# Kernel tuning notes

Measured on AMD Instinct MI355X. Metric: run time of the kernel, lower is better.

The kernel has to match this reference:

```python
import jax, jax.numpy as jnp
import numpy as np

B, L, D, KD, H = 4, 2048, 512, 64, 8


def _dequant(w_int, scale, zp):
    # per-tensor asymmetric dequantization: (q - zero_point) * scale
    return (w_int.astype(jnp.float32) - zp) * scale


def setup_inputs() -> dict:
    key = jax.random.key(0)
    ks = jax.random.split(key, 20)
    inp = {
        'query': jax.random.normal(ks[0], (B, L, D), jnp.float32),
        'key':   jax.random.normal(ks[1], (B, L, D), jnp.float32),
        'value': jax.random.normal(ks[2], (B, L, D), jnp.float32),
        'wq_q': jax.random.randint(ks[3], (D, KD, H), 0, 127, jnp.int32),
        'wk_q': jax.random.randint(ks[4], (D, KD, H), 0, 127, jnp.int32),
        'wv_q': jax.random.randint(ks[5], (D, KD, H), 0, 127, jnp.int32),
        'wo_q': jax.random.randint(ks[6], (KD * H, D), 0, 127, jnp.int32),
        'bq': jax.random.normal(ks[7], (KD, H), jnp.float32) * 0.02,
        'bk': jax.random.normal(ks[8], (KD, H), jnp.float32) * 0.02,
        'bv': jax.random.normal(ks[9], (KD, H), jnp.float32) * 0.02,
        'bo': jax.random.normal(ks[10], (D,), jnp.float32) * 0.02,
        'scale_q': jax.random.uniform(ks[11], (), jnp.float32, 0.001, 0.01),
        'scale_k': jax.random.uniform(ks[12], (), jnp.float32, 0.001, 0.01),
        'scale_v': jax.random.uniform(ks[13], (), jnp.float32, 0.001, 0.01),
        'scale_o': jax.random.uniform(ks[14], (), jnp.float32, 0.001, 0.01),
        'zp_q': jax.random.uniform(ks[15], (), jnp.float32, 50.0, 70.0),
        'zp_k': jax.random.uniform(ks[16], (), jnp.float32, 50.0, 70.0),
        'zp_v': jax.random.uniform(ks[17], (), jnp.float32, 50.0, 70.0),
        'zp_o': jax.random.uniform(ks[18], (), jnp.float32, 50.0, 70.0),
    }
    return inp


def reference(query, key, value, wq_q, wk_q, wv_q, wo_q, bq, bk, bv, bo,
              scale_q, scale_k, scale_v, scale_o, zp_q, zp_k, zp_v, zp_o):
    # Dequantize int8 weights (quantized-inference path of the layer)
    wq = _dequant(wq_q, scale_q, zp_q)  # (D, KD, H)
    wk = _dequant(wk_q, scale_k, zp_k)
    wv = _dequant(wv_q, scale_v, zp_v)
    wo = _dequant(wo_q, scale_o, zp_o)  # (KD*H, D)

    q = jnp.einsum('bij,jkh->bikh', query, wq) + bq  # (B, L, KD, H)
    k = jnp.einsum('bij,jkh->bikh', key,   wk) + bk
    v = jnp.einsum('bij,jkh->bikh', value, wv) + bv

    # scores: contract over key_dim -> (B, Lq, Lk, H)
    scores = jnp.einsum('bidh,bjdh->bijh', q, k) / jnp.sqrt(jnp.float32(KD))
    # tf softmax over axis=-2 of bikh == key axis (axis 2 here)
    attn = jax.nn.softmax(scores, axis=2)
    out = jnp.einsum('bijh,bjdh->bidh', attn, v)  # (B, L, KD, H)
    out = out.reshape(out.shape[0], out.shape[1], KD * H)  # flatten (d,h) row-major, same as tf.reshape
    return jnp.matmul(out, wo) + bo
```

## Files before the change

kernel.cpp:

```cpp
#include <hip/hip_runtime.h>
#include <math.h>
#include <stdint.h>

#define BB 4
#define LL 2048
#define DD 512
#define KDIM 64
#define HH 8

typedef _Float16 f16;
typedef f16 f16x8 __attribute__((ext_vector_type(8)));
typedef f16 f16x4v __attribute__((ext_vector_type(4)));
typedef float f32x4 __attribute__((ext_vector_type(4)));

__device__ __forceinline__ int swz(int x) { return x ^ (((x >> 7) & 7) << 4); }

__device__ __forceinline__ void gload16(const void* g, void* l) {
    __builtin_amdgcn_global_load_lds(
        (const __attribute__((address_space(1))) void*)g,
        (__attribute__((address_space(3))) void*)l, 16, 0, 0);
}

__device__ __forceinline__ void wait_barrier() {
    asm volatile("s_waitcnt vmcnt(0)" ::: "memory");
    __builtin_amdgcn_s_barrier();
}

__global__ __launch_bounds__(256)
void prep_all(const int* __restrict__ w0, const int* __restrict__ w1,
              const int* __restrict__ w2, const int* __restrict__ w3,
              const float* s0, const float* s1, const float* s2, const float* s3,
              const float* z0, const float* z1, const float* z2, const float* z3,
              f16* o0, f16* o1, f16* o2, f16* o3)
{
    __shared__ float t[32][33];
    const int zi = blockIdx.z;
    const int* W = zi == 0 ? w0 : zi == 1 ? w1 : zi == 2 ? w2 : w3;
    const float sc = *(zi == 0 ? s0 : zi == 1 ? s1 : zi == 2 ? s2 : s3);
    const float zp = *(zi == 0 ? z0 : zi == 1 ? z1 : zi == 2 ? z2 : z3);
    f16* WT = zi == 0 ? o0 : zi == 1 ? o1 : zi == 2 ? o2 : o3;
    const int n0 = blockIdx.x * 32, k0 = blockIdx.y * 32;
    const int x = threadIdx.x & 31, y = threadIdx.x >> 5;
    #pragma unroll
    for (int i = 0; i < 32; i += 8)
        t[y + i][x] = ((float)W[(size_t)(k0 + y + i) * DD + n0 + x] - zp) * sc;
    __syncthreads();
    if (zi == 3) {
        const int k = k0 + x;
        const int kp = (k & 7) * 64 + (k >> 3);
        #pragma unroll
        for (int i = 0; i < 32; i += 8)
            WT[(size_t)(n0 + y + i) * DD + kp] = (f16)t[x][y + i];
    } else {
        #pragma unroll
        for (int i = 0; i < 32; i += 8)
            WT[(size_t)(n0 + y + i) * DD + k0 + x] = (f16)t[x][y + i];
    }
}

__global__ __launch_bounds__(256)
void cast_all(const float* __restrict__ q, const float* __restrict__ k,
              const float* __restrict__ v, f16* oq, f16* ok, f16* ov)
{
    const int yi = blockIdx.y;
    const float* in = yi == 0 ? q : yi == 1 ? k : v;
    f16* out = yi == 0 ? oq : yi == 1 ? ok : ov;
    const int i = (blockIdx.x * 256 + threadIdx.x) * 4;
    float4 x = *(const float4*)(in + i);
    f16x4v o = {(f16)x.x, (f16)x.y, (f16)x.z, (f16)x.w};
    *(f16x4v*)(out + i) = o;
}

template<int EPI>
__device__ __forceinline__
void gemm_body(char* As, char* Bs, const f16* __restrict__ A,
               const f16* __restrict__ BT, const float* __restrict__ bias,
               void* __restrict__ OutP)
{
    const int tid = threadIdx.x, lane = tid & 63, wid = tid >> 6;
    const int g = lane >> 4, ql = lane & 15;
    const int wm = wid >> 1, wn = wid & 1;
    const int bid = blockIdx.x;
    const int sb = (bid & 7) * 32 + (bid >> 3);
    const int rowBase = (sb >> 2) * 128, colBase = (sb & 3) * 128;

    auto stage = [&](int p, int buf) {
        const int kt = p * 32;
        #pragma unroll
        for (int i = 0; i < 2; ++i) {
            const int xl = i * 4096 + wid * 1024 + lane * 16;
            const int xs = swz(xl);
            const int r = xs >> 6, cb = xs & 63;
            const char* asrc;
            if (EPI == 1) {
                const int m = rowBase + r, b = m >> 11, qq = m & 2047;
                const int kp = kt * 2 + cb;
                asrc = (const char*)A +
                       (((size_t)((b * 8 + (kp >> 7)) * 2048 + qq)) << 7) + (kp & 127);
            } else {
                asrc = (const char*)(A + (size_t)(rowBase + r) * DD + kt) + cb;
            }
            gload16(asrc, As + buf * 8192 + xl);
            gload16((const char*)(BT + (size_t)(colBase + r) * DD + kt) + cb,
                    Bs + buf * 8192 + xl);
        }
    };

    const f32x4 zero = {0.f, 0.f, 0.f, 0.f};
    f32x4 acc[4][4];
    #pragma unroll
    for (int i = 0; i < 4; ++i)
        #pragma unroll
        for (int j = 0; j < 4; ++j) acc[i][j] = zero;

    stage(0, 0);

    for (int p = 0; p < 16; ++p) {
        const int buf = p & 1;
        wait_barrier();
        if (p < 15) stage(p + 1, buf ^ 1);
        const char* as = As + buf * 8192;
        const char* bs = Bs + buf * 8192;
        f16x8 af[4], bf[4];
        #pragma unroll
        for (int mf = 0; mf < 4; ++mf)
            af[mf] = *(const f16x8*)(as + swz((wm * 64 + mf * 16 + ql) * 64 + g * 16));
        #pragma unroll
        for (int nf = 0; nf < 4; ++nf)
            bf[nf] = *(const f16x8*)(bs + swz((wn * 64 + nf * 16 + ql) * 64 + g * 16));
        __builtin_amdgcn_s_setprio(1);
        #pragma unroll
        for (int mf = 0; mf < 4; ++mf)
            #pragma unroll
            for (int nf = 0; nf < 4; ++nf)
                acc[mf][nf] = __builtin_amdgcn_mfma_f32_16x16x32_f16(af[mf], bf[nf], acc[mf][nf], 0, 0, 0);
        __builtin_amdgcn_s_setprio(0);
    }

    #pragma unroll
    for (int nf = 0; nf < 4; ++nf) {
        const int n = colBase + wn * 64 + nf * 16 + ql;
        const float bn = bias[n];
        #pragma unroll
        for (int mf = 0; mf < 4; ++mf) {
            const int m0 = rowBase + wm * 64 + mf * 16 + g * 4;
            if (EPI == 2) {
                const int b = m0 >> 11, l0 = m0 & 2047;
                const int kd = n >> 3, hh = n & 7;
                f16x4v o = {(f16)(acc[mf][nf][0] + bn), (f16)(acc[mf][nf][1] + bn),
                            (f16)(acc[mf][nf][2] + bn), (f16)(acc[mf][nf][3] + bn)};
                *(f16x4v*)((f16*)OutP + ((size_t)(b * HH + hh) * KDIM + kd) * LL + l0) = o;
            } else {
                #pragma unroll
                for (int r = 0; r < 4; ++r) {
                    const int m = m0 + r;
                    const float v = acc[mf][nf][r] + bn;
                    if (EPI == 0) {
                        const int b = m >> 11, lr = m & 2047;
                        const int kd = n >> 3, hh = n & 7;
                        ((f16*)OutP)[((size_t)(b * HH + hh) * LL + lr) * KDIM + kd] = (f16)v;
                    } else {
                        ((float*)OutP)[(size_t)m * DD + n] = v;
                    }
                }
            }
        }
    }
}

__global__ __launch_bounds__(256)
void gemm_qkv(const f16* Xq, const f16* Xk, const f16* Xv,
              const f16* WTq, const f16* WTk, const f16* WTv,
              const float* bq, const float* bk, const float* bv,
              f16* Qh, f16* Kh, f16* VhT)
{
    __shared__ __align__(16) char As[2 * 128 * 32 * 2];
    __shared__ __align__(16) char Bs[2 * 128 * 32 * 2];
    const int z = blockIdx.z;
    if (z == 0)      gemm_body<0>(As, Bs, Xq, WTq, bq, Qh);
    else if (z == 1) gemm_body<0>(As, Bs, Xk, WTk, bk, Kh);
    else             gemm_body<2>(As, Bs, Xv, WTv, bv, VhT);
}

__global__ __launch_bounds__(256)
void gemm_out(const f16* A, const f16* BT, const float* bias, float* Out)
{
    __shared__ __align__(16) char As[2 * 128 * 32 * 2];
    __shared__ __align__(16) char Bs[2 * 128 * 32 * 2];
    gemm_body<1>(As, Bs, A, BT, bias, Out);
}

__global__ __launch_bounds__(256, 4)
void attn_f16(const f16* __restrict__ Qh, const f16* __restrict__ Kh,
              const f16* __restrict__ VhT, f16* __restrict__ Ob)
{
    __shared__ __align__(16) char k_s[2][64 * 128];
    __shared__ __align__(16) char v_s[2][64 * 128];
    __shared__ __align__(16) char p_s[4 * 2048];

    const int tid = threadIdx.x, lane = tid & 63, wid = tid >> 6;
    const int g = lane >> 4, ql = lane & 15;
    char* pw = p_s + wid * 2048;

    const int bid = blockIdx.x;
    const int sb = (bid & 7) * 128 + (bid >> 3);
    const int qt = sb & 31, bh = sb >> 5;

    const f16*  Qb = Qh + (size_t)bh * LL * KDIM;
    const char* Kb = (const char*)(Kh + (size_t)bh * LL * KDIM);
    const char* Vb = (const char*)(VhT + (size_t)bh * KDIM * LL);
    const int q0 = qt * 64 + wid * 16;

    auto stage = [&](int t, int buf) {
        const int kv = t * 64;
        #pragma unroll
        for (int i = 0; i < 2; ++i) {
            const int xl = i * 4096 + wid * 1024 + lane * 16;
            const int xs = swz(xl);
            gload16(Kb + (size_t)kv * 128 + xs, k_s[buf] + xl);
            gload16(Vb + (size_t)(xs >> 7) * (LL * 2) + (size_t)kv * 2 + (xs & 127),
                    v_s[buf] + xl);
        }
    };

    stage(0, 0);

    const f16 qscale = (f16)(0.125f * 1.44269504089f);
    f16x8 qfr[2];
    #pragma unroll
    for (int kb = 0; kb < 2; ++kb) {
        qfr[kb] = *(const f16x8*)(Qb + (size_t)(q0 + ql) * KDIM + kb * 32 + g * 8);
        qfr[kb] *= qscale;
    }

    const f32x4 zero = {0.f, 0.f, 0.f, 0.f};
    f32x4 acc[4];
    #pragma unroll
    for (int n = 0; n < 4; ++n) acc[n] = zero;
    float m_r = -1e30f, l_r = 0.f;

    for (int t = 0; t < 32; ++t) {
        const int buf = t & 1;
        wait_barrier();
        if (t < 31) stage(t + 1, buf ^ 1);
        const char* ks = k_s[buf];
        const char* vs = v_s[buf];

        f32x4 s[4];
        __builtin_amdgcn_s_setprio(1);
        #pragma unroll
        for (int kf = 0; kf < 4; ++kf) {
            f16x8 kfr0 = *(const f16x8*)(ks + swz((kf * 16 + ql) * 128 + g * 16));
            f16x8 kfr1 = *(const f16x8*)(ks + swz((kf * 16 + ql) * 128 + 64 + g * 16));
            f32x4 z = zero;
            z = __builtin_amdgcn_mfma_f32_16x16x32_f16(kfr0, qfr[0], z, 0, 0, 0);
            z = __builtin_amdgcn_mfma_f32_16x16x32_f16(kfr1, qfr[1], z, 0, 0, 0);
            s[kf] = z;
        }
        __builtin_amdgcn_s_setprio(0);

        float mx = s[0][0];
        #pragma unroll
        for (int kf = 0; kf < 4; ++kf)
            #pragma unroll
            for (int r = 0; r < 4; ++r) mx = fmaxf(mx, s[kf][r]);
        mx = fmaxf(mx, __shfl_xor(mx, 16));
        mx = fmaxf(mx, __shfl_xor(mx, 32));
        if (__any(mx > m_r + 8.f)) {
            const float mnew = fmaxf(m_r, mx);
            const float fsc = exp2f(m_r - mnew);
            m_r = mnew;
            l_r *= fsc;
            #pragma unroll
            for (int n = 0; n < 4; ++n) acc[n] *= fsc;
        }
        float ps = 0.f;
        #pragma unroll
        for (int kf = 0; kf < 4; ++kf) {
            const float p0 = exp2f(s[kf][0] - m_r);
            const float p1 = exp2f(s[kf][1] - m_r);
            const float p2 = exp2f(s[kf][2] - m_r);
            const float p3 = exp2f(s[kf][3] - m_r);
            ps += (p0 + p1) + (p2 + p3);
            f16x4v pk = {(f16)p0, (f16)p1, (f16)p2, (f16)p3};
            *(f16x4v*)(pw + swz(ql * 128 + kf * 32 + g * 8)) = pk;
        }
        l_r += ps;

        __builtin_amdgcn_s_setprio(1);
        #pragma unroll
        for (int kb = 0; kb < 2; ++kb) {
            f16x8 pf = *(const f16x8*)(pw + swz(ql * 128 + kb * 64 + g * 16));
            #pragma unroll
            for (int n = 0; n < 4; ++n) {
                f16x8 vf = *(const f16x8*)(vs + swz((n * 16 + ql) * 128
                                                    + kb * 64 + g * 16));
                acc[n] = __builtin_amdgcn_mfma_f32_16x16x32_f16(vf, pf, acc[n], 0, 0, 0);
            }
        }
        __builtin_amdgcn_s_setprio(0);
    }

    l_r += __shfl_xor(l_r, 16);
    l_r += __shfl_xor(l_r, 32);
    const float inv = 1.f / l_r;
    const int q = q0 + ql;
    f16* orow = Ob + ((size_t)bh * LL + q) * KDIM;
    #pragma unroll
    for (int n = 0; n < 4; ++n) {
        f16x4v o = {(f16)(acc[n][0] * inv), (f16)(acc[n][1] * inv),
                    (f16)(acc[n][2] * inv), (f16)(acc[n][3] * inv)};
        *(f16x4v*)(orow + n * 16 + g * 4) = o;
    }
}

extern "C" void kernel_launch(void* const* d_in, const int* in_sizes, int n_in,
                              void* d_out, int out_size, void* d_ws, size_t ws_size,
                              hipStream_t stream)
{
    const float* query = (const float*)d_in[0];
    const float* key   = (const float*)d_in[1];
    const float* value = (const float*)d_in[2];
    const int* wq = (const int*)d_in[3];
    const int* wk = (const int*)d_in[4];
    const int* wv = (const int*)d_in[5];
    const int* wo = (const int*)d_in[6];
    const float* bq = (const float*)d_in[7];
    const float* bk = (const float*)d_in[8];
    const float* bv = (const float*)d_in[9];
    const float* bo = (const float*)d_in[10];
    const float* scale_q = (const float*)d_in[11];
    const float* scale_k = (const float*)d_in[12];
    const float* scale_v = (const float*)d_in[13];
    const float* scale_o = (const float*)d_in[14];
    const float* zp_q = (const float*)d_in[15];
    const float* zp_k = (const float*)d_in[16];
    const float* zp_v = (const float*)d_in[17];
    const float* zp_o = (const float*)d_in[18];

    const size_t MD = (size_t)BB * LL * DD;
    const size_t WT_SZ = (size_t)DD * DD;

    f16* Xq  = (f16*)d_ws;
    f16* Xk  = Xq + MD;
    f16* Xv  = Xk + MD;
    f16* WTq = Xv + MD;
    f16* WTk = WTq + WT_SZ;
    f16* WTv = WTk + WT_SZ;
    f16* WTo = WTv + WT_SZ;
    f16* Qh  = WTo + WT_SZ;
    f16* Kh  = Qh + MD;
    f16* VhT = Kh + MD;
    f16* Ob  = VhT + MD;

    dim3 gprep(16, 16, 4);
    prep_all<<<gprep, 256, 0, stream>>>(wq, wk, wv, wo,
                                        scale_q, scale_k, scale_v, scale_o,
                                        zp_q, zp_k, zp_v, zp_o,
                                        WTq, WTk, WTv, WTo);

    dim3 gcast((unsigned)(MD / 4 / 256), 3);
    cast_all<<<gcast, 256, 0, stream>>>(query, key, value, Xq, Xk, Xv);

    dim3 gg(256, 1, 3);
    gemm_qkv<<<gg, 256, 0, stream>>>(Xq, Xk, Xv, WTq, WTk, WTv,
                                     bq, bk, bv, Qh, Kh, VhT);

    attn_f16<<<1024, 256, 0, stream>>>(Qh, Kh, VhT, Ob);

    gemm_out<<<256, 256, 0, stream>>>(Ob, WTo, bo, (float*)d_out);
}
```

Measured before the change: 149.4 us.

## Merge prep/cast kernels and shrink attention blocks to two waves, single-buffered

```diff
diff --git a/kernel.cpp b/kernel.cpp
--- a/kernel.cpp
+++ b/kernel.cpp
@@ -27,48 +27,49 @@
 }
 
 __global__ __launch_bounds__(256)
-void prep_all(const int* __restrict__ w0, const int* __restrict__ w1,
+void prologue(const int* __restrict__ w0, const int* __restrict__ w1,
               const int* __restrict__ w2, const int* __restrict__ w3,
               const float* s0, const float* s1, const float* s2, const float* s3,
               const float* z0, const float* z1, const float* z2, const float* z3,
-              f16* o0, f16* o1, f16* o2, f16* o3)
+              f16* o0, f16* o1, f16* o2, f16* o3,
+              const float* __restrict__ xq, const float* __restrict__ xk,
+              const float* __restrict__ xv, f16* cq, f16* ck, f16* cv)
 {
     __shared__ float t[32][33];
-    const int zi = blockIdx.z;
-    const int* W = zi == 0 ? w0 : zi == 1 ? w1 : zi == 2 ? w2 : w3;
-    const float sc = *(zi == 0 ? s0 : zi == 1 ? s1 : zi == 2 ? s2 : s3);
-    const float zp = *(zi == 0 ? z0 : zi == 1 ? z1 : zi == 2 ? z2 : z3);
-    f16* WT = zi == 0 ? o0 : zi == 1 ? o1 : zi == 2 ? o2 : o3;
-    const int n0 = blockIdx.x * 32, k0 = blockIdx.y * 32;
-    const int x = threadIdx.x & 31, y = threadIdx.x >> 5;
-    #pragma unroll
-    for (int i = 0; i < 32; i += 8)
-        t[y + i][x] = ((float)W[(size_t)(k0 + y + i) * DD + n0 + x] - zp) * sc;
-    __syncthreads();
-    if (zi == 3) {
-        const int k = k0 + x;
-        const int kp = (k & 7) * 64 + (k >> 3);
+    const int bid = blockIdx.x;
+    if (bid < 1024) {
+        const int zi = bid >> 8, rem = bid & 255;
+        const int* W = zi == 0 ? w0 : zi == 1 ? w1 : zi == 2 ? w2 : w3;
+        const float sc = *(zi == 0 ? s0 : zi == 1 ? s1 : zi == 2 ? s2 : s3);
+        const float zp = *(zi == 0 ? z0 : zi == 1 ? z1 : zi == 2 ? z2 : z3);
+        f16* WT = zi == 0 ? o0 : zi == 1 ? o1 : zi == 2 ? o2 : o3;
+        const int n0 = (rem & 15) * 32, k0 = (rem >> 4) * 32;
+        const int x = threadIdx.x & 31, y = threadIdx.x >> 5;
         #pragma unroll
         for (int i = 0; i < 32; i += 8)
-            WT[(size_t)(n0 + y + i) * DD + kp] = (f16)t[x][y + i];
+            t[y + i][x] = ((float)W[(size_t)(k0 + y + i) * DD + n0 + x] - zp) * sc;
+        __syncthreads();
+        if (zi == 3) {
+            const int k = k0 + x;
+            const int kp = (k & 7) * 64 + (k >> 3);
+            #pragma unroll
+            for (int i = 0; i < 32; i += 8)
+                WT[(size_t)(n0 + y + i) * DD + kp] = (f16)t[x][y + i];
+        } else {
+            #pragma unroll
+            for (int i = 0; i < 32; i += 8)
+                WT[(size_t)(n0 + y + i) * DD + k0 + x] = (f16)t[x][y + i];
+        }
     } else {
-        #pragma unroll
-        for (int i = 0; i < 32; i += 8)
-            WT[(size_t)(n0 + y + i) * DD + k0 + x] = (f16)t[x][y + i];
-    }
-}
-
-__global__ __launch_bounds__(256)
-void cast_all(const float* __restrict__ q, const float* __restrict__ k,
-              const float* __restrict__ v, f16* oq, f16* ok, f16* ov)
-{
-    const int yi = blockIdx.y;
-    const float* in = yi == 0 ? q : yi == 1 ? k : v;
-    f16* out = yi == 0 ? oq : yi == 1 ? ok : ov;
-    const int i = (blockIdx.x * 256 + threadIdx.x) * 4;
-    float4 x = *(const float4*)(in + i);
-    f16x4v o = {(f16)x.x, (f16)x.y, (f16)x.z, (f16)x.w};
-    *(f16x4v*)(out + i) = o;
+        const int c = bid - 1024;
+        const int yi = c >> 12, xb = c & 4095;
+        const float* in = yi == 0 ? xq : yi == 1 ? xk : xv;
+        f16* out = yi == 0 ? cq : yi == 1 ? ck : cv;
+        const int i = (xb * 256 + threadIdx.x) * 4;
+        float4 v = *(const float4*)(in + i);
+        f16x4v o = {(f16)v.x, (f16)v.y, (f16)v.z, (f16)v.w};
+        *(f16x4v*)(out + i) = o;
+    }
 }
 
 template<int EPI>
@@ -190,40 +191,38 @@
     gemm_body<1>(As, Bs, A, BT, bias, Out);
 }
 
-__global__ __launch_bounds__(256, 4)
+__global__ __launch_bounds__(128, 4)
 void attn_f16(const f16* __restrict__ Qh, const f16* __restrict__ Kh,
               const f16* __restrict__ VhT, f16* __restrict__ Ob)
 {
-    __shared__ __align__(16) char k_s[2][64 * 128];
-    __shared__ __align__(16) char v_s[2][64 * 128];
-    __shared__ __align__(16) char p_s[4 * 2048];
+    __shared__ __align__(16) char k_s[64 * 128];
+    __shared__ __align__(16) char v_s[64 * 128];
+    __shared__ __align__(16) char p_s[2 * 2048];
 
     const int tid = threadIdx.x, lane = tid & 63, wid = tid >> 6;
     const int g = lane >> 4, ql = lane & 15;
     char* pw = p_s + wid * 2048;
 
     const int bid = blockIdx.x;
-    const int sb = (bid & 7) * 128 + (bid >> 3);
-    const int qt = sb & 31, bh = sb >> 5;
+    const int sb = (bid & 7) * 256 + (bid >> 3);
+    const int qt = sb & 63, bh = sb >> 6;
 
     const f16*  Qb = Qh + (size_t)bh * LL * KDIM;
     const char* Kb = (const char*)(Kh + (size_t)bh * LL * KDIM);
     const char* Vb = (const char*)(VhT + (size_t)bh * KDIM * LL);
-    const int q0 = qt * 64 + wid * 16;
-
-    auto stage = [&](int t, int buf) {
+    const int q0 = qt * 32 + wid * 16;
+
+    auto stage = [&](int t) {
         const int kv = t * 64;
         #pragma unroll
-        for (int i = 0; i < 2; ++i) {
-            const int xl = i * 4096 + wid * 1024 + lane * 16;
+        for (int i = 0; i < 4; ++i) {
+            const int xl = i * 2048 + wid * 1024 + lane * 16;
             const int xs = swz(xl);
-            gload16(Kb + (size_t)kv * 128 + xs, k_s[buf] + xl);
+            gload16(Kb + (size_t)kv * 128 + xs, k_s + xl);
             gload16(Vb + (size_t)(xs >> 7) * (LL * 2) + (size_t)kv * 2 + (xs & 127),
-                    v_s[buf] + xl);
+                    v_s + xl);
         }
     };
-
-    stage(0, 0);
 
     const f16 qscale = (f16)(0.125f * 1.44269504089f);
     f16x8 qfr[2];
@@ -240,18 +239,15 @@
     float m_r = -1e30f, l_r = 0.f;
 
     for (int t = 0; t < 32; ++t) {
-        const int buf = t & 1;
-        wait_barrier();
-        if (t < 31) stage(t + 1, buf ^ 1);
-        const char* ks = k_s[buf];
-        const char* vs = v_s[buf];
+        stage(t);
+        __syncthreads();
 
         f32x4 s[4];
         __builtin_amdgcn_s_setprio(1);
         #pragma unroll
         for (int kf = 0; kf < 4; ++kf) {
-            f16x8 kfr0 = *(const f16x8*)(ks + swz((kf * 16 + ql) * 128 + g * 16));
-            f16x8 kfr1 = *(const f16x8*)(ks + swz((kf * 16 + ql) * 128 + 64 + g * 16));
+            f16x8 kfr0 = *(const f16x8*)(k_s + swz((kf * 16 + ql) * 128 + g * 16));
+            f16x8 kfr1 = *(const f16x8*)(k_s + swz((kf * 16 + ql) * 128 + 64 + g * 16));
             f32x4 z = zero;
             z = __builtin_amdgcn_mfma_f32_16x16x32_f16(kfr0, qfr[0], z, 0, 0, 0);
             z = __builtin_amdgcn_mfma_f32_16x16x32_f16(kfr1, qfr[1], z, 0, 0, 0);
@@ -259,11 +255,13 @@
         }
         __builtin_amdgcn_s_setprio(0);
 
-        float mx = s[0][0];
-        #pragma unroll
-        for (int kf = 0; kf < 4; ++kf)
-            #pragma unroll
-            for (int r = 0; r < 4; ++r) mx = fmaxf(mx, s[kf][r]);
+        float a0 = fmaxf(fmaxf(s[0][0], s[0][1]), s[0][2]);
+        float a1 = fmaxf(fmaxf(s[0][3], s[1][0]), s[1][1]);
+        float a2 = fmaxf(fmaxf(s[1][2], s[1][3]), s[2][0]);
+        float a3 = fmaxf(fmaxf(s[2][1], s[2][2]), s[2][3]);
+        float a4 = fmaxf(fmaxf(s[3][0], s[3][1]), s[3][2]);
+        float mx = fmaxf(fmaxf(fmaxf(a0, a1), fmaxf(a2, a3)),
+                         fmaxf(a4, s[3][3]));
         mx = fmaxf(mx, __shfl_xor(mx, 16));
         mx = fmaxf(mx, __shfl_xor(mx, 32));
         if (__any(mx > m_r + 8.f)) {
@@ -293,12 +291,13 @@
             f16x8 pf = *(const f16x8*)(pw + swz(ql * 128 + kb * 64 + g * 16));
             #pragma unroll
             for (int n = 0; n < 4; ++n) {
-                f16x8 vf = *(const f16x8*)(vs + swz((n * 16 + ql) * 128
-                                                    + kb * 64 + g * 16));
+                f16x8 vf = *(const f16x8*)(v_s + swz((n * 16 + ql) * 128
+                                                     + kb * 64 + g * 16));
                 acc[n] = __builtin_amdgcn_mfma_f32_16x16x32_f16(vf, pf, acc[n], 0, 0, 0);
             }
         }
         __builtin_amdgcn_s_setprio(0);
+        __syncthreads();
     }
 
     l_r += __shfl_xor(l_r, 16);
@@ -353,20 +352,16 @@
     f16* VhT = Kh + MD;
     f16* Ob  = VhT + MD;
 
-    dim3 gprep(16, 16, 4);
-    prep_all<<<gprep, 256, 0, stream>>>(wq, wk, wv, wo,
-                                        scale_q, scale_k, scale_v, scale_o,
-                                        zp_q, zp_k, zp_v, zp_o,
-                                        WTq, WTk, WTv, WTo);
-
-    dim3 gcast((unsigned)(MD / 4 / 256), 3);
-    cast_all<<<gcast, 256, 0, stream>>>(query, key, value, Xq, Xk, Xv);
+    prologue<<<1024 + 3 * 4096, 256, 0, stream>>>(
+        wq, wk, wv, wo, scale_q, scale_k, scale_v, scale_o,
+        zp_q, zp_k, zp_v, zp_o, WTq, WTk, WTv, WTo,
+        query, key, value, Xq, Xk, Xv);
 
     dim3 gg(256, 1, 3);
     gemm_qkv<<<gg, 256, 0, stream>>>(Xq, Xk, Xv, WTq, WTk, WTv,
                                      bq, bk, bv, Qh, Kh, VhT);
 
-    attn_f16<<<1024, 256, 0, stream>>>(Qh, Kh, VhT, Ob);
+    attn_f16<<<2048, 128, 0, stream>>>(Qh, Kh, VhT, Ob);
 
     gemm_out<<<256, 256, 0, stream>>>(Ob, WTo, bo, (float*)d_out);
 }
```

After: 157.0 us. +5.1%, slower.
